# Performance work log

Hardware: AMD Instinct MI355X
Metric: run time of the kernel (lower is better)

## Reference

```python
import jax, jax.numpy as jnp
import numpy as np

T, H = 4096, 7168          # tokens, hidden size
Q_LORA, KV_LORA = 1536, 512
ROPE, NOPE, NH = 64, 128, 16
QK = NOPE + ROPE
MAXPOS, SLOTS = 8192, 16384
EPS = 1e-6


def _build_cos_sin_cache():
    # rotary cache layout used by the module: [max_pos, rope] = cos_half || sin_half
    half = ROPE // 2
    inv_freq = 1.0 / (10000.0 ** (np.arange(0, half, dtype=np.float32) / half))
    t = np.arange(MAXPOS, dtype=np.float32)
    freqs = np.outer(t, inv_freq)  # [MAXPOS, half]
    return jnp.asarray(np.concatenate([np.cos(freqs), np.sin(freqs)], axis=-1))


def setup_inputs() -> dict:
    key = jax.random.key(0)
    ks = jax.random.split(key, 8)
    return {
        "hidden_states": jax.random.normal(ks[0], (T, H), jnp.float32),
        "positions": jax.random.randint(ks[1], (T,), 0, MAXPOS, jnp.int32),
        "w_qkv_a": jax.random.normal(ks[2], (H, Q_LORA + KV_LORA + ROPE), jnp.float32) * 0.02,
        "q_a_ln_w": jnp.ones((Q_LORA,), jnp.float32),
        "w_q_b": jax.random.normal(ks[3], (Q_LORA, NH * QK), jnp.float32) * 0.02,
        "kv_a_ln_w": jnp.ones((KV_LORA,), jnp.float32),
        "w_kc": jax.random.normal(ks[4], (NH, NOPE, KV_LORA), jnp.float32) * 0.02,
        "cos_sin_cache": _build_cos_sin_cache(),
        "k_cache": jnp.zeros((SLOTS, KV_LORA), jnp.float32),
        "rope_cache": jnp.zeros((SLOTS, ROPE), jnp.float32),
        "slot_mapping": jnp.arange(T, dtype=jnp.int32),
    }


def _rms_norm(x, w, eps=EPS):
    return x * jax.lax.rsqrt(jnp.mean(x * x, axis=-1, keepdims=True) + eps) * w


def _interleave_rope(x, cos, sin):
    # npu_interleave_rope: de-interleave even/odd lanes into halves, then
    # apply neox-style rotation with full-dim (repeated) cos/sin.
    x1 = x[..., 0::2]
    x2 = x[..., 1::2]
    rot = jnp.concatenate([x1, x2], axis=-1)
    h = rot.shape[-1] // 2
    rot_half = jnp.concatenate([-rot[..., h:], rot[..., :h]], axis=-1)
    return rot * cos + rot_half * sin


def reference(hidden_states, positions, w_qkv_a, q_a_ln_w, w_q_b, kv_a_ln_w,
              w_kc, cos_sin_cache, k_cache, rope_cache, slot_mapping):
    # get_sin_cos: gather cache, chunk in halves, repeat each to full rope dim
    cs = cos_sin_cache[positions]                 # [T, ROPE]
    cos, sin = jnp.split(cs, 2, axis=-1)          # [T, ROPE/2] each
    cos = jnp.tile(cos, (1, 2))                   # [T, ROPE]
    sin = jnp.tile(sin, (1, 2))

    # fused qkv_a projection -> q low-rank + latent kv cache
    qkv = hidden_states @ w_qkv_a                 # [T, Q_LORA + KV_LORA + ROPE]
    q_low = qkv[:, :Q_LORA]
    latent = qkv[:, Q_LORA:]

    # q path: RMSNorm -> q_b projection -> per-head split
    q = _rms_norm(q_low, q_a_ln_w)
    q = (q @ w_q_b).reshape(-1, NH, QK)           # [T, NH, QK]
    q_nope, q_pe = q[..., :NOPE], q[..., NOPE:]

    # absorb: q_nope @ w_kc per head -> [T, NH, KV_LORA]
    q_nope = jnp.einsum("thn,hnk->thk", q_nope, w_kc)
    # interleaved rope on q_pe
    q_pe = _interleave_rope(q_pe, cos[:, None, :], sin[:, None, :])

    # kv path (npu_kv_rmsnorm_rope_cache): rmsnorm latent, rope the rope part,
    # scatter both into the paged caches at slot_mapping
    k_nope = _rms_norm(latent[:, :KV_LORA], kv_a_ln_w)     # [T, KV_LORA]
    k_rope = _interleave_rope(latent[:, KV_LORA:], cos, sin)  # [T, ROPE]
    k_cache = k_cache.at[slot_mapping].set(k_nope)
    rope_cache = rope_cache.at[slot_mapping].set(k_rope)

    q_out = jnp.concatenate([q_nope, q_pe], axis=-1)       # [T, NH, KV_LORA+ROPE]
    k_out = jnp.concatenate([k_nope, k_rope], axis=-1)     # [T, KV_LORA+ROPE]
    return q_out, k_out, k_cache, rope_cache
```

## Files before the change

kernel.cpp:

```cpp
#include <hip/hip_runtime.h>
#include <hip/hip_bf16.h>

typedef __bf16 bf16_t;
typedef __bf16 bf16x4 __attribute__((ext_vector_type(4)));
typedef __bf16 bf16x8 __attribute__((ext_vector_type(8)));
typedef float f32x4 __attribute__((ext_vector_type(4)));
typedef unsigned int uint;

#define T_TOK 4096
#define H_DIM 7168
#define QLORA 1536
#define KVLORA 512
#define ROPE_D 64
#define NOPE_D 128
#define NHEAD 16
#define NQKV 2112
#define NQB  3072
#define EPS_F 1e-6f


__device__ inline void transpose_tile64(const float* __restrict__ in,
                                        bf16_t* __restrict__ out,
                                        int R, int C, int bx, int by,
                                        float (*tile)[65])
{
    const int tx = threadIdx.x & 15, ty = threadIdx.x >> 4;
    #pragma unroll
    for (int i = 0; i < 4; i++) {
        const int r = ty + 16 * i;
        const float4 v = *(const float4*)&in[(long)(by + r) * C + bx + tx * 4];
        tile[r][tx * 4 + 0] = v.x; tile[r][tx * 4 + 1] = v.y;
        tile[r][tx * 4 + 2] = v.z; tile[r][tx * 4 + 3] = v.w;
    }
    __syncthreads();
    #pragma unroll
    for (int i = 0; i < 4; i++) {
        const int cc = ty + 16 * i;
        bf16x4 o;
        o[0] = (bf16_t)tile[tx * 4 + 0][cc];
        o[1] = (bf16_t)tile[tx * 4 + 1][cc];
        o[2] = (bf16_t)tile[tx * 4 + 2][cc];
        o[3] = (bf16_t)tile[tx * 4 + 3][cc];
        *(bf16x4*)&out[(long)(bx + cc) * R + by + tx * 4] = o;
    }
}

__global__ __launch_bounds__(256) void preamble_kernel(
    const float* __restrict__ hs, const float* __restrict__ w_qkv_a,
    const float* __restrict__ w_q_b, const float* __restrict__ w_kc,
    bf16_t* __restrict__ hs_bf, bf16_t* __restrict__ wqkvaT,
    bf16_t* __restrict__ wqbT, bf16_t* __restrict__ wkcT)
{
    __shared__ float tile[64][65];
    const int b = blockIdx.x;
    if (b < 3696) {
        transpose_tile64(w_qkv_a, wqkvaT, H_DIM, NQKV, (b % 33) * 64, (b / 33) * 64, tile);
    } else if (b < 4848) {
        const int i = b - 3696;
        transpose_tile64(w_q_b, wqbT, QLORA, NQB, (i % 48) * 64, (i / 48) * 64, tile);
    } else if (b < 5104) {
        const int i = b - 4848;
        transpose_tile64(w_kc, wkcT, 2048, 512, (i % 8) * 64, (i / 8) * 64, tile);
    } else {
        const int i = b - 5104;
        const long n8 = (long)T_TOK * H_DIM / 8;
        const long stride = 1024L * 256;
        for (long idx = (long)i * 256 + threadIdx.x; idx < n8; idx += stride) {
            const float4 a = ((const float4*)hs)[idx * 2];
            const float4 c = ((const float4*)hs)[idx * 2 + 1];
            bf16x8 v;
            v[0] = (bf16_t)a.x; v[1] = (bf16_t)a.y; v[2] = (bf16_t)a.z; v[3] = (bf16_t)a.w;
            v[4] = (bf16_t)c.x; v[5] = (bf16_t)c.y; v[6] = (bf16_t)c.z; v[7] = (bf16_t)c.w;
            ((bf16x8*)hs_bf)[idx] = v;
        }
    }
}

__device__ inline float block_sum_256(float v)
{
    #pragma unroll
    for (int off = 32; off > 0; off >>= 1) v += __shfl_xor(v, off, 64);
    __shared__ float tmp[4];
    __syncthreads();
    if ((threadIdx.x & 63) == 0) tmp[threadIdx.x >> 6] = v;
    __syncthreads();
    return tmp[0] + tmp[1] + tmp[2] + tmp[3];
}

__global__ __launch_bounds__(256) void rmsq_kside_kernel(
    const float* __restrict__ qkv, const float* __restrict__ qB,
    const float* __restrict__ q_w, const float* __restrict__ kv_w,
    const float* __restrict__ cos_sin, const int* __restrict__ positions,
    const int* __restrict__ slot_map,
    bf16_t* __restrict__ q_a, float* __restrict__ k_out,
    float* __restrict__ kc_out, float* __restrict__ rc_out)
{
    const int t = blockIdx.x;
    const long base = (long)t * NQKV;
    const float* x = qkv + base;
    const float* xB = qB ? qB + base : nullptr;

    float loc[6];
    float ss = 0.f;
    #pragma unroll
    for (int i = 0; i < 6; i++) {
        int idx = threadIdx.x + 256 * i;
        float v = x[idx];
        if (xB) v += xB[idx];
        loc[i] = v; ss += v * v;
    }
    ss = block_sum_256(ss);
    const float scq = rsqrtf(ss / (float)QLORA + EPS_F);
    #pragma unroll
    for (int i = 0; i < 6; i++) {
        int idx = threadIdx.x + 256 * i;
        q_a[(long)t * QLORA + idx] = (bf16_t)(loc[i] * scq * q_w[idx]);
    }

    float v0 = x[QLORA + threadIdx.x];
    float v1 = x[QLORA + threadIdx.x + 256];
    if (xB) { v0 += xB[QLORA + threadIdx.x]; v1 += xB[QLORA + threadIdx.x + 256]; }
    float ssk = v0 * v0 + v1 * v1;
    ssk = block_sum_256(ssk);
    const float sck = rsqrtf(ssk / (float)KVLORA + EPS_F);
    const int slot = slot_map[t];
    const float a0 = v0 * sck * kv_w[threadIdx.x];
    const float a1 = v1 * sck * kv_w[threadIdx.x + 256];
    k_out[(long)t * 576 + threadIdx.x]        = a0;
    k_out[(long)t * 576 + 256 + threadIdx.x]  = a1;
    kc_out[(long)slot * KVLORA + threadIdx.x]       = a0;
    kc_out[(long)slot * KVLORA + 256 + threadIdx.x] = a1;
    if (threadIdx.x < 32) {
        const int j = threadIdx.x;
        const int pos = positions[t];
        const float c = cos_sin[pos * 64 + j];
        const float s = cos_sin[pos * 64 + 32 + j];
        float x1 = x[QLORA + KVLORA + 2 * j];
        float x2 = x[QLORA + KVLORA + 2 * j + 1];
        if (xB) { x1 += xB[QLORA + KVLORA + 2 * j]; x2 += xB[QLORA + KVLORA + 2 * j + 1]; }
        const float o1 = x1 * c - x2 * s;
        const float o2 = x2 * c + x1 * s;
        k_out[(long)t * 576 + 512 + j]      = o1;
        k_out[(long)t * 576 + 512 + 32 + j] = o2;
        rc_out[(long)slot * 64 + j]      = o1;
        rc_out[(long)slot * 64 + 32 + j] = o2;
    }
}

#define GBM 128
#define GBN 128
#define GBK 64

#define KSPLIT_TILE_COMPUTE(aa, bb)                                                          \
    bf16x8 a0, a1, a2, a3, b0, b1, b2, b3;                                                   \
    asm volatile("ds_read_b128 %0, %1 offset:0"    : "=v"(a0) : "v"(aa));                    \
    asm volatile("ds_read_b128 %0, %1 offset:2048" : "=v"(a1) : "v"(aa));                    \
    asm volatile("ds_read_b128 %0, %1 offset:4096" : "=v"(a2) : "v"(aa));                    \
    asm volatile("ds_read_b128 %0, %1 offset:6144" : "=v"(a3) : "v"(aa));                    \
    asm volatile("ds_read_b128 %0, %1 offset:0"    : "=v"(b0) : "v"(bb));                    \
    asm volatile("ds_read_b128 %0, %1 offset:2048" : "=v"(b1) : "v"(bb));                    \
    asm volatile("ds_read_b128 %0, %1 offset:4096" : "=v"(b2) : "v"(bb));                    \
    asm volatile("ds_read_b128 %0, %1 offset:6144" : "=v"(b3) : "v"(bb));                    \
    asm volatile("s_waitcnt lgkmcnt(0)" ::: "memory");                                       \
    __builtin_amdgcn_sched_barrier(0);                                                       \
    __builtin_amdgcn_s_setprio(1);                                                           \
    acc[0][0] = __builtin_amdgcn_mfma_f32_16x16x32_bf16(a0, b0, acc[0][0], 0, 0, 0);         \
    acc[0][1] = __builtin_amdgcn_mfma_f32_16x16x32_bf16(a0, b1, acc[0][1], 0, 0, 0);         \
    acc[0][2] = __builtin_amdgcn_mfma_f32_16x16x32_bf16(a0, b2, acc[0][2], 0, 0, 0);         \
    acc[0][3] = __builtin_amdgcn_mfma_f32_16x16x32_bf16(a0, b3, acc[0][3], 0, 0, 0);         \
    acc[1][0] = __builtin_amdgcn_mfma_f32_16x16x32_bf16(a1, b0, acc[1][0], 0, 0, 0);         \
    acc[1][1] = __builtin_amdgcn_mfma_f32_16x16x32_bf16(a1, b1, acc[1][1], 0, 0, 0);         \
    acc[1][2] = __builtin_amdgcn_mfma_f32_16x16x32_bf16(a1, b2, acc[1][2], 0, 0, 0);         \
    acc[1][3] = __builtin_amdgcn_mfma_f32_16x16x32_bf16(a1, b3, acc[1][3], 0, 0, 0);         \
    acc[2][0] = __builtin_amdgcn_mfma_f32_16x16x32_bf16(a2, b0, acc[2][0], 0, 0, 0);         \
    acc[2][1] = __builtin_amdgcn_mfma_f32_16x16x32_bf16(a2, b1, acc[2][1], 0, 0, 0);         \
    acc[2][2] = __builtin_amdgcn_mfma_f32_16x16x32_bf16(a2, b2, acc[2][2], 0, 0, 0);         \
    acc[2][3] = __builtin_amdgcn_mfma_f32_16x16x32_bf16(a2, b3, acc[2][3], 0, 0, 0);         \
    acc[3][0] = __builtin_amdgcn_mfma_f32_16x16x32_bf16(a3, b0, acc[3][0], 0, 0, 0);         \
    acc[3][1] = __builtin_amdgcn_mfma_f32_16x16x32_bf16(a3, b1, acc[3][1], 0, 0, 0);         \
    acc[3][2] = __builtin_amdgcn_mfma_f32_16x16x32_bf16(a3, b2, acc[3][2], 0, 0, 0);         \
    acc[3][3] = __builtin_amdgcn_mfma_f32_16x16x32_bf16(a3, b3, acc[3][3], 0, 0, 0);         \
    __builtin_amdgcn_s_setprio(0);

__global__ __launch_bounds__(512, 4) void gemm_mfma(
    const bf16_t* __restrict__ A, int lda, long sA,
    const bf16_t* __restrict__ Bt, int ldb, long sB,
    float* __restrict__ C, int ldc, long sC,
    int K, int N)
{
    __shared__ bf16_t As[2][GBM * GBK];
    __shared__ bf16_t Bs[2][GBN * GBK];

    const int nwg = gridDim.x * gridDim.y;
    const int bid = blockIdx.y * gridDim.x + blockIdx.x;
    const int cpx = nwg >> 3;
    const int swz = (bid & 7) * cpx + (bid >> 3);
    const int bx = swz % gridDim.x;
    const int by = swz / gridDim.x;

    const int tid = threadIdx.x;
    const int lane = tid & 63;
    const int w = tid >> 6;
    const int q = w >> 1;
    const int p = w & 1;
    const int qr = q >> 1, qc = q & 1;
    const int fr = lane & 15;
    const int kg = lane >> 4;

    const long brow = (long)by * GBM;
    const long bcol = (long)bx * GBN;

    const bf16_t* Ab = A + blockIdx.z * sA + brow * lda;
    const bf16_t* Bb = Bt + blockIdx.z * sB;
    float* Cb = C + blockIdx.z * sC + brow * ldc;

    const int srow = w * 16 + (lane >> 3);
    const int scol = (((lane & 7) ^ (lane >> 3)) * 8);

    const uint rd_sw = (uint)(((kg * 16) ^ ((fr & 7) << 4)) ^ (p << 6));
    const uint a_base = (uint)(uintptr_t)(&As[0][0]) + (uint)((qr * 64 + fr) * 128) + rd_sw;
    const uint b_base = (uint)(uintptr_t)(&Bs[0][0]) + (uint)((qc * 64 + fr) * 128) + rd_sw;

    f32x4 acc[4][4] = {};

    const int nt = K / GBK;

    auto stage = [&](int buf, int k0) {
        #pragma unroll
        for (int it = 0; it < 2; it++) {
            const int r = srow + it * 8;
            __builtin_amdgcn_global_load_lds(
                (const __attribute__((address_space(1))) void*)(Ab + (long)r * lda + k0 + scol),
                (__attribute__((address_space(3))) void*)(&As[buf][(w * 16 + it * 8) * GBK]),
                16, 0, 0);
        }
        #pragma unroll
        for (int it = 0; it < 2; it++) {
            const int r = srow + it * 8;
            long bn = bcol + r; if (bn >= N) bn = N - 1;
            __builtin_amdgcn_global_load_lds(
                (const __attribute__((address_space(1))) void*)(Bb + bn * ldb + k0 + scol),
                (__attribute__((address_space(3))) void*)(&Bs[buf][(w * 16 + it * 8) * GBK]),
                16, 0, 0);
        }
    };

    stage(0, 0);
    asm volatile("s_waitcnt vmcnt(0)" ::: "memory");
    __builtin_amdgcn_s_barrier();

    int cur = 0;
    for (int t = 0; t < nt; ++t) {
        if (t + 1 < nt) stage(cur ^ 1, (t + 1) * GBK);

        const uint aa = a_base + (uint)(cur * (GBM * GBK * 2));
        const uint bb = b_base + (uint)(cur * (GBN * GBK * 2));
        { KSPLIT_TILE_COMPUTE(aa, bb) }

        asm volatile("s_waitcnt vmcnt(0)" ::: "memory");
        __builtin_amdgcn_s_barrier();
        cur ^= 1;
    }

    float* red = (q < 2) ? (float*)&As[0][0] : (float*)&Bs[0][0];
    red += (q & 1) * 4096;
    if (p == 1) {
        #pragma unroll
        for (int i = 0; i < 4; i++)
            #pragma unroll
            for (int j = 0; j < 4; j++)
                *(f32x4*)&red[(i * 4 + j) * 256 + lane * 4] = acc[i][j];
    }
    __syncthreads();
    if (p == 0) {
        #pragma unroll
        for (int i = 0; i < 4; i++) {
            #pragma unroll
            for (int j = 0; j < 4; j++) {
                acc[i][j] += *(const f32x4*)&red[(i * 4 + j) * 256 + lane * 4];
                const int row0 = qr * 64 + i * 16 + kg * 4;
                const long col = bcol + qc * 64 + j * 16 + fr;
                if (col < N) {
                    #pragma unroll
                    for (int r = 0; r < 4; r++)
                        Cb[(long)(row0 + r) * ldc + col] = acc[i][j][r];
                }
            }
        }
    }
}

__global__ __launch_bounds__(512, 4) void gemm2_fused(
    const bf16_t* __restrict__ A,
    const bf16_t* __restrict__ Bt,
    const float* __restrict__ cos_sin,
    const int* __restrict__ positions,
    bf16_t* __restrict__ q_nope,
    float* __restrict__ q_out)
{
    __shared__ bf16_t As[2][GBM * GBK];
    __shared__ bf16_t Bs[2][GBN * GBK];

    const int nwg = gridDim.x * gridDim.y;
    const int bid = blockIdx.y * gridDim.x + blockIdx.x;
    const int cpx = nwg >> 3;
    const int swz = (bid & 7) * cpx + (bid >> 3);
    const int bx = swz % gridDim.x;
    const int by = swz / gridDim.x;

    const int tid = threadIdx.x;
    const int lane = tid & 63;
    const int w = tid >> 6;
    const int q = w >> 1;
    const int p = w & 1;
    const int qr = q >> 1, qc = q & 1;
    const int fr = lane & 15;
    const int kg = lane >> 4;

    const int brow = by * GBM;
    const int bcol = bx * GBN;

    const bf16_t* Ab = A + (long)brow * QLORA;
    const bf16_t* Bb = Bt + (long)bcol * QLORA;

    const int srow = w * 16 + (lane >> 3);
    const int scol = (((lane & 7) ^ (lane >> 3)) * 8);

    const uint rd_sw = (uint)(((kg * 16) ^ ((fr & 7) << 4)) ^ (p << 6));
    const uint a_base = (uint)(uintptr_t)(&As[0][0]) + (uint)((qr * 64 + fr) * 128) + rd_sw;
    const uint b_base = (uint)(uintptr_t)(&Bs[0][0]) + (uint)((qc * 64 + fr) * 128) + rd_sw;

    f32x4 acc[4][4] = {};

    const int nt = QLORA / GBK;

    auto stage = [&](int buf, int k0) {
        #pragma unroll
        for (int it = 0; it < 2; it++) {
            const int r = srow + it * 8;
            __builtin_amdgcn_global_load_lds(
                (const __attribute__((address_space(1))) void*)(Ab + (long)r * QLORA + k0 + scol),
                (__attribute__((address_space(3))) void*)(&As[buf][(w * 16 + it * 8) * GBK]),
                16, 0, 0);
            __builtin_amdgcn_global_load_lds(
                (const __attribute__((address_space(1))) void*)(Bb + (long)r * QLORA + k0 + scol),
                (__attribute__((address_space(3))) void*)(&Bs[buf][(w * 16 + it * 8) * GBK]),
                16, 0, 0);
        }
    };

    stage(0, 0);
    asm volatile("s_waitcnt vmcnt(0)" ::: "memory");
    __builtin_amdgcn_s_barrier();

    int cur = 0;
    for (int t = 0; t < nt; ++t) {
        if (t + 1 < nt) stage(cur ^ 1, (t + 1) * GBK);

        const uint aa = a_base + (uint)(cur * (GBM * GBK * 2));
        const uint bb = b_base + (uint)(cur * (GBN * GBK * 2));
        { KSPLIT_TILE_COMPUTE(aa, bb) }

        asm volatile("s_waitcnt vmcnt(0)" ::: "memory");
        __builtin_amdgcn_s_barrier();
        cur ^= 1;
    }

    float* red = (q < 2) ? (float*)&As[0][0] : (float*)&Bs[0][0];
    red += (q & 1) * 4096;
    if (p == 1) {
        #pragma unroll
        for (int i = 0; i < 4; i++)
            #pragma unroll
            for (int j = 0; j < 4; j++)
                *(f32x4*)&red[(i * 4 + j) * 256 + lane * 4] = acc[i][j];
    }
    __syncthreads();
    if (p == 0) {
        #pragma unroll
        for (int i = 0; i < 4; i++) {
            #pragma unroll
            for (int j = 0; j < 4; j++) {
                acc[i][j] += *(const f32x4*)&red[(i * 4 + j) * 256 + lane * 4];
                const int row0 = qr * 64 + i * 16 + kg * 4;
                const int col  = bcol + qc * 64 + j * 16 + fr;
                const int h  = col / 192;
                const int jj = col - h * 192;
                if (jj < 128) {
                    #pragma unroll
                    for (int r = 0; r < 4; r++) {
                        const int t = brow + row0 + r;
                        q_nope[((long)h * T_TOK + t) * NOPE_D + jj] = (bf16_t)acc[i][j][r];
                    }
                } else {
                    const int idx = jj - 128;
                    const int j2 = idx >> 1;
                    const int odd = idx & 1;
                    #pragma unroll
                    for (int r = 0; r < 4; r++) {
                        const int t = brow + row0 + r;
                        const float v = acc[i][j][r];
                        const float pr = __shfl_xor(v, 1, 64);
                        const int pos = positions[t];
                        const float c = cos_sin[pos * 64 + j2];
                        const float s = cos_sin[pos * 64 + 32 + j2];
                        const float o = odd ? (v * c + pr * s) : (v * c - pr * s);
                        q_out[(long)t * 9216 + h * 576 + 512 + (odd ? 32 : 0) + j2] = o;
                    }
                }
            }
        }
    }
}

__global__ __launch_bounds__(512) void gemm3_k128(
    const bf16_t* __restrict__ A,
    const bf16_t* __restrict__ Bt,
    float* __restrict__ C)
{
    __shared__ bf16_t As[2][GBM * GBK];
    __shared__ bf16_t Bs[2][GBN * GBK];

    const int nwg = gridDim.x * gridDim.y;
    const int bid = blockIdx.y * gridDim.x + blockIdx.x;
    const int cpx = nwg >> 3;
    const int swz = (bid & 7) * cpx + (bid >> 3);
    const int bx = swz % gridDim.x;
    const int by = swz / gridDim.x;

    const int tid = threadIdx.x;
    const int lane = tid & 63;
    const int w = tid >> 6;
    const int wr = w >> 2, wc = w & 3;
    const int fr = lane & 15;
    const int kg = lane >> 4;

    const long brow = (long)by * GBM;
    const long bcol = (long)bx * GBN;

    const bf16_t* Ab = A + (long)blockIdx.z * T_TOK * NOPE_D + brow * NOPE_D;
    const bf16_t* Bb = Bt + blockIdx.z * 128;
    float* Cb = C + blockIdx.z * 576 + brow * 9216;

    const int srow = w * 16 + (lane >> 3);
    const int scol = (((lane & 7) ^ (lane >> 3)) * 8);

    const uint rd_sw = (uint)((kg * 16) ^ ((fr & 7) << 4));

    #pragma unroll
    for (int kh = 0; kh < 2; kh++) {
        #pragma unroll
        for (int it = 0; it < 2; it++) {
            const int r = srow + it * 8;
            __builtin_amdgcn_global_load_lds(
                (const __attribute__((address_space(1))) void*)(Ab + (long)r * NOPE_D + kh * 64 + scol),
                (__attribute__((address_space(3))) void*)(&As[kh][(w * 16 + it * 8) * GBK]),
                16, 0, 0);
        }
        #pragma unroll
        for (int it = 0; it < 2; it++) {
            const int r = srow + it * 8;
            __builtin_amdgcn_global_load_lds(
                (const __attribute__((address_space(1))) void*)(Bb + (bcol + r) * 2048 + kh * 64 + scol),
                (__attribute__((address_space(3))) void*)(&Bs[kh][(w * 16 + it * 8) * GBK]),
                16, 0, 0);
        }
    }
    asm volatile("s_waitcnt vmcnt(0)" ::: "memory");
    __builtin_amdgcn_s_barrier();

    f32x4 acc[4][2] = {};

    #pragma unroll
    for (int kh = 0; kh < 2; kh++) {
        const uint aa  = (uint)(uintptr_t)(&As[kh][0]) + (uint)((wr * 64 + fr) * 128) + rd_sw;
        const uint bb  = (uint)(uintptr_t)(&Bs[kh][0]) + (uint)((wc * 32 + fr) * 128) + rd_sw;
        const uint aaX = aa ^ 64u;
        const uint bbX = bb ^ 64u;
        bf16x8 a00, a01, a02, a03, a10, a11, a12, a13, b00, b01, b10, b11;
        asm volatile("ds_read_b128 %0, %1 offset:0"    : "=v"(a00) : "v"(aa));
        asm volatile("ds_read_b128 %0, %1 offset:2048" : "=v"(a01) : "v"(aa));
        asm volatile("ds_read_b128 %0, %1 offset:4096" : "=v"(a02) : "v"(aa));
        asm volatile("ds_read_b128 %0, %1 offset:6144" : "=v"(a03) : "v"(aa));
        asm volatile("ds_read_b128 %0, %1 offset:0"    : "=v"(a10) : "v"(aaX));
        asm volatile("ds_read_b128 %0, %1 offset:2048" : "=v"(a11) : "v"(aaX));
        asm volatile("ds_read_b128 %0, %1 offset:4096" : "=v"(a12) : "v"(aaX));
        asm volatile("ds_read_b128 %0, %1 offset:6144" : "=v"(a13) : "v"(aaX));
        asm volatile("ds_read_b128 %0, %1 offset:0"    : "=v"(b00) : "v"(bb));
        asm volatile("ds_read_b128 %0, %1 offset:2048" : "=v"(b01) : "v"(bb));
        asm volatile("ds_read_b128 %0, %1 offset:0"    : "=v"(b10) : "v"(bbX));
        asm volatile("ds_read_b128 %0, %1 offset:2048" : "=v"(b11) : "v"(bbX));
        asm volatile("s_waitcnt lgkmcnt(0)" ::: "memory");
        __builtin_amdgcn_sched_barrier(0);

        __builtin_amdgcn_s_setprio(1);
        acc[0][0] = __builtin_amdgcn_mfma_f32_16x16x32_bf16(a00, b00, acc[0][0], 0, 0, 0);
        acc[0][1] = __builtin_amdgcn_mfma_f32_16x16x32_bf16(a00, b01, acc[0][1], 0, 0, 0);
        acc[1][0] = __builtin_amdgcn_mfma_f32_16x16x32_bf16(a01, b00, acc[1][0], 0, 0, 0);
        acc[1][1] = __builtin_amdgcn_mfma_f32_16x16x32_bf16(a01, b01, acc[1][1], 0, 0, 0);
        acc[2][0] = __builtin_amdgcn_mfma_f32_16x16x32_bf16(a02, b00, acc[2][0], 0, 0, 0);
        acc[2][1] = __builtin_amdgcn_mfma_f32_16x16x32_bf16(a02, b01, acc[2][1], 0, 0, 0);
        acc[3][0] = __builtin_amdgcn_mfma_f32_16x16x32_bf16(a03, b00, acc[3][0], 0, 0, 0);
        acc[3][1] = __builtin_amdgcn_mfma_f32_16x16x32_bf16(a03, b01, acc[3][1], 0, 0, 0);
        acc[0][0] = __builtin_amdgcn_mfma_f32_16x16x32_bf16(a10, b10, acc[0][0], 0, 0, 0);
        acc[0][1] = __builtin_amdgcn_mfma_f32_16x16x32_bf16(a10, b11, acc[0][1], 0, 0, 0);
        acc[1][0] = __builtin_amdgcn_mfma_f32_16x16x32_bf16(a11, b10, acc[1][0], 0, 0, 0);
        acc[1][1] = __builtin_amdgcn_mfma_f32_16x16x32_bf16(a11, b11, acc[1][1], 0, 0, 0);
        acc[2][0] = __builtin_amdgcn_mfma_f32_16x16x32_bf16(a12, b10, acc[2][0], 0, 0, 0);
        acc[2][1] = __builtin_amdgcn_mfma_f32_16x16x32_bf16(a12, b11, acc[2][1], 0, 0, 0);
        acc[3][0] = __builtin_amdgcn_mfma_f32_16x16x32_bf16(a13, b10, acc[3][0], 0, 0, 0);
        acc[3][1] = __builtin_amdgcn_mfma_f32_16x16x32_bf16(a13, b11, acc[3][1], 0, 0, 0);
        __builtin_amdgcn_s_setprio(0);
    }

    #pragma unroll
    for (int i = 0; i < 4; i++) {
        #pragma unroll
        for (int j = 0; j < 2; j++) {
            const int row0 = wr * 64 + i * 16 + kg * 4;
            const long col = bcol + wc * 32 + j * 16 + fr;
            #pragma unroll
            for (int r = 0; r < 4; r++)
                Cb[(long)(row0 + r) * 9216 + col] = acc[i][j][r];
        }
    }
}


extern "C" void kernel_launch(void* const* d_in, const int* in_sizes, int n_in,
                              void* d_out, int out_size, void* d_ws, size_t ws_size,
                              hipStream_t stream)
{
    const float* hs       = (const float*)d_in[0];
    const int*   positions= (const int*)d_in[1];
    const float* w_qkv_a  = (const float*)d_in[2];
    const float* q_a_ln_w = (const float*)d_in[3];
    const float* w_q_b    = (const float*)d_in[4];
    const float* kv_a_ln_w= (const float*)d_in[5];
    const float* w_kc     = (const float*)d_in[6];
    const float* cos_sin  = (const float*)d_in[7];
    const float* k_cache_in  = (const float*)d_in[8];
    const float* rope_cache_in = (const float*)d_in[9];
    const int*   slot_map = (const int*)d_in[10];

    float* out   = (float*)d_out;
    float* q_out = out;
    float* k_out = out + 37748736;
    float* kc_out = out + 40108032;
    float* rc_out = out + 48496640;

    char* ws = (char*)d_ws;
    bf16_t* hs_bf  = (bf16_t*)(ws + 0);
    bf16_t* wqkvaT = (bf16_t*)(ws + 58720256);
    bf16_t* wqbT   = (bf16_t*)(ws + 88997888);
    bf16_t* wkcT   = (bf16_t*)(ws + 98435072);
    float*  qkv0   = (float*)(ws + 100532224);

    const bool splitk = ws_size >= (size_t)169738240;

    float* qkv1 = nullptr;
    bf16_t* q_a;
    bf16_t* q_nope;
    if (splitk) {
        qkv1   = (float*)(ws + 135135232);
        q_a    = (bf16_t*)(ws + 0);
        q_nope = (bf16_t*)(ws + 135135232);
    } else {
        q_a    = (bf16_t*)(ws + 135135232);
        q_nope = (bf16_t*)(ws + 100532224);
    }

    hipMemcpyAsync(kc_out, k_cache_in, (size_t)16384 * 512 * 4, hipMemcpyDeviceToDevice, stream);
    hipMemcpyAsync(rc_out, rope_cache_in, (size_t)16384 * 64 * 4, hipMemcpyDeviceToDevice, stream);

    preamble_kernel<<<6128, 256, 0, stream>>>(hs, w_qkv_a, w_q_b, w_kc,
                                              hs_bf, wqkvaT, wqbT, wkcT);

    if (splitk) {
        gemm_mfma<<<dim3((NQKV + GBN - 1) / GBN, T_TOK / GBM, 2), 512, 0, stream>>>(
            hs_bf, H_DIM, 3584, wqkvaT, H_DIM, 3584,
            qkv0, NQKV, (long)T_TOK * NQKV, 3584, NQKV);
    } else {
        gemm_mfma<<<dim3((NQKV + GBN - 1) / GBN, T_TOK / GBM, 1), 512, 0, stream>>>(
            hs_bf, H_DIM, 0, wqkvaT, H_DIM, 0, qkv0, NQKV, 0, H_DIM, NQKV);
    }

    rmsq_kside_kernel<<<T_TOK, 256, 0, stream>>>(qkv0, qkv1, q_a_ln_w, kv_a_ln_w,
                                                 cos_sin, positions, slot_map,
                                                 q_a, k_out, kc_out, rc_out);

    gemm2_fused<<<dim3(NQB / GBN, T_TOK / GBM), 512, 0, stream>>>(
        q_a, wqbT, cos_sin, positions, q_nope, q_out);

    gemm3_k128<<<dim3(KVLORA / GBN, T_TOK / GBM, NHEAD), 512, 0, stream>>>(
        q_nope, wkcT, q_out);
}
```

Measured before the change: 352.4 us.

## Fold cache copies into preamble kernel and vectorize RMSNorm kernel

Removes the two device-to-device hipMemcpyAsync calls for the k and rope caches and does those copies inside the preamble kernel with 1024 extra blocks using float4 loads and stores. The aim is to save launch and serialization overhead and let the copies overlap with the weight transposes and bf16 casts. The RMSNorm/k-side kernel is also rewritten to use float4 loads and stores and bf16x4 stores in place of scalar accesses. The cost is that the copy blocks now compete with the transpose work inside one grid.

```diff
diff --git a/kernel.cpp b/kernel.cpp
--- a/kernel.cpp
+++ b/kernel.cpp
@@ -48,8 +48,10 @@
 __global__ __launch_bounds__(256) void preamble_kernel(
     const float* __restrict__ hs, const float* __restrict__ w_qkv_a,
     const float* __restrict__ w_q_b, const float* __restrict__ w_kc,
+    const float* __restrict__ k_cache_in, const float* __restrict__ rope_cache_in,
     bf16_t* __restrict__ hs_bf, bf16_t* __restrict__ wqkvaT,
-    bf16_t* __restrict__ wqbT, bf16_t* __restrict__ wkcT)
+    bf16_t* __restrict__ wqbT, bf16_t* __restrict__ wkcT,
+    float* __restrict__ kc_out, float* __restrict__ rc_out)
 {
     __shared__ float tile[64][65];
     const int b = blockIdx.x;
@@ -61,7 +63,7 @@
     } else if (b < 5104) {
         const int i = b - 4848;
         transpose_tile64(w_kc, wkcT, 2048, 512, (i % 8) * 64, (i / 8) * 64, tile);
-    } else {
+    } else if (b < 6128) {
         const int i = b - 5104;
         const long n8 = (long)T_TOK * H_DIM / 8;
         const long stride = 1024L * 256;
@@ -73,6 +75,15 @@
             v[4] = (bf16_t)c.x; v[5] = (bf16_t)c.y; v[6] = (bf16_t)c.z; v[7] = (bf16_t)c.w;
             ((bf16x8*)hs_bf)[idx] = v;
         }
+    } else {
+        const int i = b - 6128;
+        const long nkc = 2097152;
+        const long ntot = 2359296;
+        const long stride = 1024L * 256;
+        for (long idx = (long)i * 256 + threadIdx.x; idx < ntot; idx += stride) {
+            if (idx < nkc) ((float4*)kc_out)[idx] = ((const float4*)k_cache_in)[idx];
+            else ((float4*)rc_out)[idx - nkc] = ((const float4*)rope_cache_in)[idx - nkc];
+        }
     }
 }
 
@@ -96,48 +107,63 @@
     float* __restrict__ kc_out, float* __restrict__ rc_out)
 {
     const int t = blockIdx.x;
+    const int tx = threadIdx.x;
     const long base = (long)t * NQKV;
-    const float* x = qkv + base;
-    const float* xB = qB ? qB + base : nullptr;
-
-    float loc[6];
-    float ss = 0.f;
-    #pragma unroll
-    for (int i = 0; i < 6; i++) {
-        int idx = threadIdx.x + 256 * i;
-        float v = x[idx];
-        if (xB) v += xB[idx];
-        loc[i] = v; ss += v * v;
-    }
+    const float4* x4 = (const float4*)(qkv + base);
+    const float4* xB4 = qB ? (const float4*)(qB + base) : nullptr;
+
+    float4 va = x4[tx];
+    if (xB4) { const float4 bb = xB4[tx]; va.x += bb.x; va.y += bb.y; va.z += bb.z; va.w += bb.w; }
+    float4 vb = make_float4(0.f, 0.f, 0.f, 0.f);
+    if (tx < 128) {
+        vb = x4[256 + tx];
+        if (xB4) { const float4 bb = xB4[256 + tx]; vb.x += bb.x; vb.y += bb.y; vb.z += bb.z; vb.w += bb.w; }
+    }
+    float ss = va.x * va.x + va.y * va.y + va.z * va.z + va.w * va.w
+             + vb.x * vb.x + vb.y * vb.y + vb.z * vb.z + vb.w * vb.w;
     ss = block_sum_256(ss);
     const float scq = rsqrtf(ss / (float)QLORA + EPS_F);
-    #pragma unroll
-    for (int i = 0; i < 6; i++) {
-        int idx = threadIdx.x + 256 * i;
-        q_a[(long)t * QLORA + idx] = (bf16_t)(loc[i] * scq * q_w[idx]);
-    }
-
-    float v0 = x[QLORA + threadIdx.x];
-    float v1 = x[QLORA + threadIdx.x + 256];
-    if (xB) { v0 += xB[QLORA + threadIdx.x]; v1 += xB[QLORA + threadIdx.x + 256]; }
-    float ssk = v0 * v0 + v1 * v1;
+    {
+        const float4 w0 = ((const float4*)q_w)[tx];
+        bf16x4 o;
+        o[0] = (bf16_t)(va.x * scq * w0.x); o[1] = (bf16_t)(va.y * scq * w0.y);
+        o[2] = (bf16_t)(va.z * scq * w0.z); o[3] = (bf16_t)(va.w * scq * w0.w);
+        *(bf16x4*)&q_a[(long)t * QLORA + tx * 4] = o;
+        if (tx < 128) {
+            const float4 w1 = ((const float4*)q_w)[256 + tx];
+            bf16x4 o1;
+            o1[0] = (bf16_t)(vb.x * scq * w1.x); o1[1] = (bf16_t)(vb.y * scq * w1.y);
+            o1[2] = (bf16_t)(vb.z * scq * w1.z); o1[3] = (bf16_t)(vb.w * scq * w1.w);
+            *(bf16x4*)&q_a[(long)t * QLORA + (256 + tx) * 4] = o1;
+        }
+    }
+
+    float4 kv = make_float4(0.f, 0.f, 0.f, 0.f);
+    if (tx < 128) {
+        kv = x4[384 + tx];
+        if (xB4) { const float4 bb = xB4[384 + tx]; kv.x += bb.x; kv.y += bb.y; kv.z += bb.z; kv.w += bb.w; }
+    }
+    float ssk = kv.x * kv.x + kv.y * kv.y + kv.z * kv.z + kv.w * kv.w;
     ssk = block_sum_256(ssk);
     const float sck = rsqrtf(ssk / (float)KVLORA + EPS_F);
     const int slot = slot_map[t];
-    const float a0 = v0 * sck * kv_w[threadIdx.x];
-    const float a1 = v1 * sck * kv_w[threadIdx.x + 256];
-    k_out[(long)t * 576 + threadIdx.x]        = a0;
-    k_out[(long)t * 576 + 256 + threadIdx.x]  = a1;
-    kc_out[(long)slot * KVLORA + threadIdx.x]       = a0;
-    kc_out[(long)slot * KVLORA + 256 + threadIdx.x] = a1;
-    if (threadIdx.x < 32) {
-        const int j = threadIdx.x;
+    if (tx < 128) {
+        const float4 wv = ((const float4*)kv_w)[tx];
+        float4 a;
+        a.x = kv.x * sck * wv.x; a.y = kv.y * sck * wv.y;
+        a.z = kv.z * sck * wv.z; a.w = kv.w * sck * wv.w;
+        *(float4*)&k_out[(long)t * 576 + tx * 4] = a;
+        *(float4*)&kc_out[(long)slot * KVLORA + tx * 4] = a;
+    }
+    if (tx < 32) {
+        const int j = tx;
         const int pos = positions[t];
         const float c = cos_sin[pos * 64 + j];
         const float s = cos_sin[pos * 64 + 32 + j];
+        const float* x = qkv + base;
         float x1 = x[QLORA + KVLORA + 2 * j];
         float x2 = x[QLORA + KVLORA + 2 * j + 1];
-        if (xB) { x1 += xB[QLORA + KVLORA + 2 * j]; x2 += xB[QLORA + KVLORA + 2 * j + 1]; }
+        if (qB) { x1 += qB[base + QLORA + KVLORA + 2 * j]; x2 += qB[base + QLORA + KVLORA + 2 * j + 1]; }
         const float o1 = x1 * c - x2 * s;
         const float o2 = x2 * c + x1 * s;
         k_out[(long)t * 576 + 512 + j]      = o1;
@@ -570,11 +596,10 @@
         q_nope = (bf16_t*)(ws + 100532224);
     }
 
-    hipMemcpyAsync(kc_out, k_cache_in, (size_t)16384 * 512 * 4, hipMemcpyDeviceToDevice, stream);
-    hipMemcpyAsync(rc_out, rope_cache_in, (size_t)16384 * 64 * 4, hipMemcpyDeviceToDevice, stream);
-
-    preamble_kernel<<<6128, 256, 0, stream>>>(hs, w_qkv_a, w_q_b, w_kc,
-                                              hs_bf, wqkvaT, wqbT, wkcT);
+    preamble_kernel<<<7152, 256, 0, stream>>>(hs, w_qkv_a, w_q_b, w_kc,
+                                              k_cache_in, rope_cache_in,
+                                              hs_bf, wqkvaT, wqbT, wkcT,
+                                              kc_out, rc_out);
 
     if (splitk) {
         gemm_mfma<<<dim3((NQKV + GBN - 1) / GBN, T_TOK / GBM, 2), 512, 0, stream>>>(
```

New measurement: 356.5 us. No clear change (+1.2%).
